# Kernel optimization log

Hardware: AMD Instinct MI355X
Metric: run time of the kernel (lower is better)

Reference implementation:

```python
import jax, jax.numpy as jnp
import numpy as np

D = 160          # volume side
WIN = 32         # spatial window size (box filter, matches fftconvolve with ones kernel)
NUM_MIN = 100    # minimum count constraint (constraint.min_number_from_ratio)
K_CCL = 16       # fixed number of 6-neighbor min-propagation sweeps (CCL definition)
NUM_BINS = 4096  # fixed histogram bins replacing data-dependent np.unique
VALUES = (0, 1, 2)
LIST_LABELS = (1,)
NUM_LABELS = 2
HALF = WIN // 2


def _box1d(x, w, ax):
    # 'same' box-sum along one axis via cumsum (== fftconvolve with ones(w))
    left = w // 2
    right = w - 1 - left
    x = jnp.moveaxis(x, ax, -1)
    pads = [(0, 0)] * (x.ndim - 1) + [(left, right)]
    c = jnp.cumsum(jnp.pad(x, pads), axis=-1)
    c = jnp.pad(c, [(0, 0)] * (x.ndim - 1) + [(1, 0)])
    out = c[..., w:] - c[..., :-w]
    return jnp.moveaxis(out, -1, ax)


def box_sum(x, w):
    for ax in range(x.ndim):
        x = _box1d(x, w, ax)
    return x


def _shift(a, s, ax, fill):
    # shift by s along ax, filling vacated border with `fill`
    r = jnp.roll(a, s, axis=ax)
    n = a.shape[ax]
    co = jnp.arange(n).reshape([n if i == ax else 1 for i in range(a.ndim)])
    bad = (co < s) if s > 0 else (co >= n + s)
    return jnp.where(bad, fill, r)


def label_size_map(seg):
    # create_label_size_map: connected-component labeling (6-connectivity,
    # K_CCL min-propagation sweeps) then replace each component by its size.
    n_vox = seg.size
    big = jnp.int32(n_vox + 2)
    idx = (jnp.arange(n_vox, dtype=jnp.int32) + 1).reshape(seg.shape)
    lab0 = jnp.where(seg, idx, big)

    def step(_, lab):
        m = lab
        for ax in range(seg.ndim):
            for s in (1, -1):
                m = jnp.minimum(m, _shift(lab, s, ax, big))
        return jnp.where(seg, m, big)

    lab = jax.lax.fori_loop(0, K_CCL, step, lab0)
    labels = jnp.where(seg, lab, 0)  # background -> label 0
    cnt = jnp.zeros(n_vox + 1, jnp.float32).at[labels.ravel()].add(1.0)
    return jnp.where(seg, cnt[labels], 0.0)


def _proba_weights(candidates, mean_list):
    # create_probability_weights: reciprocal-histogram weighting over rounded
    # mean component sizes (fixed NUM_BINS integer bins; bin 0 = non-candidate).
    pw = jnp.ones_like(candidates)
    for m in mean_list:
        possible = candidates * m
        idx = jnp.clip(jnp.round(possible), 0, NUM_BINS - 1).astype(jnp.int32)
        hist = jnp.zeros(NUM_BINS, jnp.float32).at[idx.ravel()].add(1.0)
        numb = jnp.sum(hist[1:])
        rec = jnp.where(hist[1:] > 0, numb / jnp.maximum(hist[1:], 1.0), 0.0)
        ph = rec / jnp.sum(rec)
        ph_full = jnp.concatenate([jnp.zeros(1, jnp.float32), ph])
        pw = pw * ph_full[idx]
    return pw / jnp.sum(pw)


def setup_inputs() -> dict:
    key = jax.random.key(0)
    data = jax.random.randint(key, (D, D, D), 0, 3).astype(jnp.float32)
    return {"data": data}


def reference(data):
    data = jnp.round(data)
    inner = tuple(s - 2 * HALF for s in data.shape)
    final = jnp.pad(jnp.ones(inner, jnp.float32), [(HALF, HALF)] * 3)
    mean_list = []
    valid_others = []
    for v in VALUES:
        seg = data == v
        segf = seg.astype(jnp.float32)
        lsize = label_size_map(seg)
        cw = box_sum(segf, WIN)                              # counts_window
        valid = (cw > max(NUM_MIN, 1)).astype(jnp.float32)   # valid_places
        cs = box_sum(lsize * valid, WIN)                     # counts_size
        mean = jnp.where(cw > 0, cs / jnp.maximum(cw, 1.0), 0.0)
        if v in LIST_LABELS:
            mean_list.append(mean)
            final = final * valid
        else:
            valid_others.append(valid)
    for vo in valid_others:
        final = final + vo
    num_labels_add = max(NUM_LABELS - len(LIST_LABELS), 0)
    candidates = (final >= num_labels_add + 1).astype(jnp.float32)
    proba_fin = _proba_weights(candidates, mean_list)
    return candidates, proba_fin
```

## Files before the change

kernel.cpp:

```cpp
#include <hip/hip_runtime.h>
#include <cmath>

#define D 160
#define DD (D*D)
#define NVOX (D*D*D)
#define BIGV (NVOX + 2)
#define NBINS 4096
#define HALF 16
#define RGRID 800
#define SGRID 1000
#define NSWEEP 16

template<int MODE>
__global__ __launch_bounds__(256) void box_rot_int_kernel(
    const void* __restrict__ vin, unsigned* __restrict__ out)
{
    __shared__ unsigned tin[32][161];
    __shared__ unsigned filt[160][33];
    int L0 = blockIdx.x * 32;
    size_t base = (size_t)L0 * D;

    if (MODE == 0) {
        const float4* s4 = (const float4*)((const float*)vin + base);
        for (int i = threadIdx.x; i < 32 * (D / 4); i += 256) {
            float4 v = s4[i];
            int e = i * 4, r = e / D, c = e - r * D;
            float rr;
            rr = rintf(v.x); tin[r][c]   = (rr==0.f) | ((rr==1.f)?0x10000u:0u);
            rr = rintf(v.y); tin[r][c+1] = (rr==0.f) | ((rr==1.f)?0x10000u:0u);
            rr = rintf(v.z); tin[r][c+2] = (rr==0.f) | ((rr==1.f)?0x10000u:0u);
            rr = rintf(v.w); tin[r][c+3] = (rr==0.f) | ((rr==1.f)?0x10000u:0u);
        }
    } else {
        const uint4* s4 = (const uint4*)((const unsigned*)vin + base);
        for (int i = threadIdx.x; i < 32 * (D / 4); i += 256) {
            uint4 v = s4[i];
            int e = i * 4, r = e / D, c = e - r * D;
            tin[r][c] = v.x; tin[r][c+1] = v.y; tin[r][c+2] = v.z; tin[r][c+3] = v.w;
        }
    }
    __syncthreads();

    {
        int r = threadIdx.x & 31, s = threadIdx.x >> 5;
        int i0 = 20 * s;
        const unsigned* ln = tin[r];
        unsigned sum = 0u;
        int jlo = i0 - 16; if (jlo < 0) jlo = 0;
        int jhi = i0 + 15; if (jhi > D - 1) jhi = D - 1;
        for (int j = jlo; j <= jhi; ++j) sum += ln[j];
        #pragma unroll 4
        for (int k = 0; k < 20; ++k) {
            int i = i0 + k;
            filt[i][r] = sum;
            int add = i + 16, rem = i - 16;
            if (add <= D - 1) sum += ln[add];
            if (rem >= 0)     sum -= ln[rem];
        }
    }
    __syncthreads();

    int r = threadIdx.x & 31;
    for (int c = (threadIdx.x >> 5); c < D; c += 8)
        out[(size_t)c * DD + L0 + r] = filt[c][r];
}

__global__ __launch_bounds__(256) void box_rot_f32_g_kernel(
    const int* __restrict__ lab, const int* __restrict__ cnt,
    const unsigned* __restrict__ cwp, float* __restrict__ out)
{
    __shared__ float tin[32][161];
    __shared__ float filt[160][33];
    int L0 = blockIdx.x * 32;
    size_t base = (size_t)L0 * D;

    const int4*  lab4 = (const int4*)(lab + base);
    const uint4* cw4  = (const uint4*)(cwp + base);
    for (int i = threadIdx.x; i < 32 * (D / 4); i += 256) {
        int4 l = lab4[i];
        uint4 cw = cw4[i];
        int e = i * 4, r = e / D, c = e - r * D;
        tin[r][c]   = (l.x != BIGV && (cw.x >> 16) > 100u) ? (float)cnt[l.x] : 0.f;
        tin[r][c+1] = (l.y != BIGV && (cw.y >> 16) > 100u) ? (float)cnt[l.y] : 0.f;
        tin[r][c+2] = (l.z != BIGV && (cw.z >> 16) > 100u) ? (float)cnt[l.z] : 0.f;
        tin[r][c+3] = (l.w != BIGV && (cw.w >> 16) > 100u) ? (float)cnt[l.w] : 0.f;
    }
    __syncthreads();

    {
        int r = threadIdx.x & 31, s = threadIdx.x >> 5;
        int i0 = 20 * s;
        const float* ln = tin[r];
        float sum = 0.f;
        int jlo = i0 - 16; if (jlo < 0) jlo = 0;
        int jhi = i0 + 15; if (jhi > D - 1) jhi = D - 1;
        for (int j = jlo; j <= jhi; ++j) sum += ln[j];
        #pragma unroll 4
        for (int k = 0; k < 20; ++k) {
            int i = i0 + k;
            filt[i][r] = sum;
            int add = i + 16, rem = i - 16;
            if (add <= D - 1) sum += ln[add];
            if (rem >= 0)     sum -= ln[rem];
        }
    }
    __syncthreads();

    int r = threadIdx.x & 31;
    for (int c = (threadIdx.x >> 5); c < D; c += 8)
        out[(size_t)c * DD + L0 + r] = filt[c][r];
}

__global__ __launch_bounds__(256) void box_rot_f32_kernel(
    const float* __restrict__ fin, float* __restrict__ out)
{
    __shared__ float tin[32][161];
    __shared__ float filt[160][33];
    int L0 = blockIdx.x * 32;
    size_t base = (size_t)L0 * D;

    const float4* s4 = (const float4*)(fin + base);
    for (int i = threadIdx.x; i < 32 * (D / 4); i += 256) {
        float4 v = s4[i];
        int e = i * 4, r = e / D, c = e - r * D;
        tin[r][c] = v.x; tin[r][c+1] = v.y; tin[r][c+2] = v.z; tin[r][c+3] = v.w;
    }
    __syncthreads();

    {
        int r = threadIdx.x & 31, s = threadIdx.x >> 5;
        int i0 = 20 * s;
        const float* ln = tin[r];
        float sum = 0.f;
        int jlo = i0 - 16; if (jlo < 0) jlo = 0;
        int jhi = i0 + 15; if (jhi > D - 1) jhi = D - 1;
        for (int j = jlo; j <= jhi; ++j) sum += ln[j];
        #pragma unroll 4
        for (int k = 0; k < 20; ++k) {
            int i = i0 + k;
            filt[i][r] = sum;
            int add = i + 16, rem = i - 16;
            if (add <= D - 1) sum += ln[add];
            if (rem >= 0)     sum -= ln[rem];
        }
    }
    __syncthreads();

    int r = threadIdx.x & 31;
    for (int c = (threadIdx.x >> 5); c < D; c += 8)
        out[(size_t)c * DD + L0 + r] = filt[c][r];
}

__global__ __launch_bounds__(256) void box_rot_fin_kernel(
    const float* __restrict__ fin, const unsigned* __restrict__ cwp,
    float* __restrict__ cand, unsigned short* __restrict__ idxbuf,
    int* __restrict__ partial)
{
    __shared__ float tin[32][161];
    __shared__ float filt[160][33];
    __shared__ int lh[NBINS];
    for (int i = threadIdx.x; i < NBINS; i += 256) lh[i] = 0;

    int L0 = blockIdx.x * 32;
    size_t base = (size_t)L0 * D;
    const float4* s4 = (const float4*)(fin + base);
    for (int i = threadIdx.x; i < 32 * (D / 4); i += 256) {
        float4 v = s4[i];
        int e = i * 4, r = e / D, c = e - r * D;
        tin[r][c] = v.x; tin[r][c+1] = v.y; tin[r][c+2] = v.z; tin[r][c+3] = v.w;
    }
    __syncthreads();

    {
        int r = threadIdx.x & 31, s = threadIdx.x >> 5;
        int i0 = 20 * s;
        const float* ln = tin[r];
        float sum = 0.f;
        int jlo = i0 - 16; if (jlo < 0) jlo = 0;
        int jhi = i0 + 15; if (jhi > D - 1) jhi = D - 1;
        for (int j = jlo; j <= jhi; ++j) sum += ln[j];
        #pragma unroll 4
        for (int k = 0; k < 20; ++k) {
            int i = i0 + k;
            filt[i][r] = sum;
            int add = i + 16, rem = i - 16;
            if (add <= D - 1) sum += ln[add];
            if (rem >= 0)     sum -= ln[rem];
        }
    }
    __syncthreads();

    int r = threadIdx.x & 31;
    int L = L0 + r;
    int y = L / D, z = L - (L / D) * D;
    bool byz = (y >= HALF && y < D - HALF && z >= HALF && z < D - HALF);
    int wy = min(y + 15, D - 1) - max(y - 16, 0) + 1;
    int wz = min(z + 15, D - 1) - max(z - 16, 0) + 1;
    for (int c = (threadIdx.x >> 5); c < D; c += 8) {
        int p = c * DD + L;
        unsigned pk = cwp[p];
        unsigned cw0 = pk & 0xFFFFu;
        unsigned cw1 = pk >> 16;
        int wx = min(c + 15, D - 1) - max(c - 16, 0) + 1;
        unsigned cw2 = (unsigned)(wx * wy * wz) - cw0 - cw1;
        float v0 = (cw0 > 100u) ? 1.f : 0.f;
        float v1 = (cw1 > 100u) ? 1.f : 0.f;
        float v2 = (cw2 > 100u) ? 1.f : 0.f;
        float border = (byz && c >= HALF && c < D - HALF) ? 1.f : 0.f;
        float cd = (border * v1 + v0 + v2 >= 2.f) ? 1.f : 0.f;
        cand[p] = cd;
        float mean = (cw1 > 0u) ? filt[c][r] / fmaxf((float)cw1, 1.f) : 0.f;
        int idx = (int)rintf(cd * mean);
        idx = min(max(idx, 0), NBINS - 1);
        idxbuf[p] = (unsigned short)idx;
        if (idx != 0) atomicAdd(&lh[idx], 1);
    }
    __syncthreads();
    int* po = partial + blockIdx.x * NBINS;
    for (int i = threadIdx.x; i < NBINS; i += 256) po[i] = lh[i];
}

__device__ __forceinline__ int min6(int c, int a, int b, int d, int e, int f, int g) {
    if (c == BIGV) return BIGV;
    return min(min(min(c, a), min(b, d)), min(min(e, f), g));
}

__device__ __forceinline__ void wave_count(int l, int lane, int* __restrict__ cnt) {
    unsigned long long remaining = __ballot(l != BIGV);
    while (remaining) {
        int leader = __ffsll((unsigned long long)remaining) - 1;
        int ll = __shfl(l, leader, 64);
        unsigned long long mm = __ballot(l == ll);
        if (lane == leader) atomicAdd(&cnt[ll], (int)__popcll(mm & remaining));
        remaining &= ~mm;
    }
}

__device__ __forceinline__ int4 cls4(float4 v, int p0) {
    int4 l;
    l.x = (rintf(v.x) == 1.f) ? (p0 + 1) : BIGV;
    l.y = (rintf(v.y) == 1.f) ? (p0 + 2) : BIGV;
    l.z = (rintf(v.z) == 1.f) ? (p0 + 3) : BIGV;
    l.w = (rintf(v.w) == 1.f) ? (p0 + 4) : BIGV;
    return l;
}

#define SWEEP_CHUNK(c, lm, rm, q, p, LOAD4, outv)                         \
    {                                                                     \
        int rr = (p) / D;                                                 \
        int yy = rr % D;                                                  \
        int xx = rr / D;                                                  \
        int4 yl = BIG4, yh = BIG4, xl = BIG4, xh = BIG4;                  \
        if (yy > 0)     yl = LOAD4((q) - D/4,  (p) - D);                  \
        if (yy < D - 1) yh = LOAD4((q) + D/4,  (p) + D);                  \
        if (xx > 0)     xl = LOAD4((q) - DD/4, (p) - DD);                 \
        if (xx < D - 1) xh = LOAD4((q) + DD/4, (p) + DD);                 \
        outv.x = min6(c.x, lm,  c.y, yl.x, yh.x, xl.x, xh.x);             \
        outv.y = min6(c.y, c.x, c.z, yl.y, yh.y, xl.y, xh.y);             \
        outv.z = min6(c.z, c.y, c.w, yl.z, yh.z, xl.z, xh.z);             \
        outv.w = min6(c.w, c.z, rm,  yl.w, yh.w, xl.w, xh.w);             \
    }

__global__ __launch_bounds__(512) void ccl_sweep1_data_kernel(
    const float* __restrict__ data, int* __restrict__ outp)
{
    int b = blockIdx.x;
    int sb = (b & 7) * (SGRID / 8) + (b >> 3);
    int lane = threadIdx.x & 63;
    int wv   = threadIdx.x >> 6;
    int wbase = sb * 4096 + wv * 512;
    int pA = wbase + 4 * lane;
    int pB = pA + 256;
    int qA = pA >> 2, qB = pB >> 2;
    const float4* d4 = (const float4*)data;
    int4 cA = cls4(d4[qA], pA), cB = cls4(d4[qB], pB);

    int zA = pA % D, zB = pB % D;
    int lmA = __shfl_up(cA.w, 1);
    int rmA = __shfl_down(cA.x, 1);
    int lmB = __shfl_up(cB.w, 1);
    int rmB = __shfl_down(cB.x, 1);
    int stA = __shfl(cB.x, 0, 64);
    int stB = __shfl(cA.w, 63, 64);
    if (lane == 63) rmA = stA;
    if (lane == 0)  lmB = stB;
    if (zA == 0)          lmA = BIGV;
    else if (lane == 0)   lmA = (rintf(data[pA - 1]) == 1.f) ? pA : BIGV;
    if (zA == D - 4)      rmA = BIGV;
    if (zB == 0)          lmB = BIGV;
    if (zB == D - 4)      rmB = BIGV;
    else if (lane == 63)  rmB = (rintf(data[pB + 4]) == 1.f) ? (pB + 5) : BIGV;

    const int4 BIG4 = make_int4(BIGV, BIGV, BIGV, BIGV);
    #define LOADD(qq, pp) cls4(d4[(qq)], (pp))
    int4 oA, oB;
    SWEEP_CHUNK(cA, lmA, rmA, qA, pA, LOADD, oA);
    SWEEP_CHUNK(cB, lmB, rmB, qB, pB, LOADD, oB);
    #undef LOADD

    int4* out4 = (int4*)outp;
    out4[qA] = oA; out4[qB] = oB;
}

template<int COUNT>
__global__ __launch_bounds__(512) void ccl_sweep8_kernel(
    const int* __restrict__ lab, int* __restrict__ outp, int* __restrict__ cnt)
{
    int b = blockIdx.x;
    int sb = (b & 7) * (SGRID / 8) + (b >> 3);
    int lane = threadIdx.x & 63;
    int wv   = threadIdx.x >> 6;
    int wbase = sb * 4096 + wv * 512;
    int pA = wbase + 4 * lane;
    int pB = pA + 256;
    int qA = pA >> 2, qB = pB >> 2;
    const int4* lab4 = (const int4*)lab;
    int4 cA = lab4[qA], cB = lab4[qB];

    int zA = pA % D, zB = pB % D;
    int lmA = __shfl_up(cA.w, 1);
    int rmA = __shfl_down(cA.x, 1);
    int lmB = __shfl_up(cB.w, 1);
    int rmB = __shfl_down(cB.x, 1);
    int stA = __shfl(cB.x, 0, 64);
    int stB = __shfl(cA.w, 63, 64);
    if (lane == 63) rmA = stA;
    if (lane == 0)  lmB = stB;
    if (zA == 0)          lmA = BIGV;
    else if (lane == 0)   lmA = lab[pA - 1];
    if (zA == D - 4)      rmA = BIGV;
    if (zB == 0)          lmB = BIGV;
    if (zB == D - 4)      rmB = BIGV;
    else if (lane == 63)  rmB = lab[pB + 4];

    const int4 BIG4 = make_int4(BIGV, BIGV, BIGV, BIGV);
    #define LOADL(qq, pp) lab4[(qq)]
    int4 oA, oB;
    SWEEP_CHUNK(cA, lmA, rmA, qA, pA, LOADL, oA);
    SWEEP_CHUNK(cB, lmB, rmB, qB, pB, LOADL, oB);
    #undef LOADL

    int4* out4 = (int4*)outp;
    out4[qA] = oA; out4[qB] = oB;

    if (COUNT) {
        wave_count(oA.x, lane, cnt);
        wave_count(oA.y, lane, cnt);
        wave_count(oA.z, lane, cnt);
        wave_count(oA.w, lane, cnt);
        wave_count(oB.x, lane, cnt);
        wave_count(oB.y, lane, cnt);
        wave_count(oB.z, lane, cnt);
        wave_count(oB.w, lane, cnt);
    }
}

__global__ __launch_bounds__(256) void hist_reduce_kernel(
    const int* __restrict__ partial, int* __restrict__ hist)
{
    int bin = blockIdx.x * 256 + threadIdx.x;
    int s = 0;
    #pragma unroll 4
    for (int b = 0; b < RGRID; ++b) s += partial[b * NBINS + bin];
    hist[bin] = s;
}

__global__ __launch_bounds__(256) void hist_post_kernel(
    const int* __restrict__ hist, float* __restrict__ ph_full,
    float* __restrict__ Sout)
{
    __shared__ float red[256];
    int t = threadIdx.x;

    float loc = 0.f;
    for (int b = t; b < NBINS; b += 256)
        if (b >= 1) loc += (float)hist[b];
    red[t] = loc; __syncthreads();
    for (int o = 128; o > 0; o >>= 1) { if (t < o) red[t] += red[t + o]; __syncthreads(); }
    float numb = red[0]; __syncthreads();

    loc = 0.f;
    for (int b = t; b < NBINS; b += 256) {
        float r = 0.f;
        if (b >= 1) {
            int h = hist[b];
            if (h > 0) r = numb / (float)h;
        }
        ph_full[b] = r;
        loc += r;
    }
    red[t] = loc; __syncthreads();
    for (int o = 128; o > 0; o >>= 1) { if (t < o) red[t] += red[t + o]; __syncthreads(); }
    float sumrec = red[0]; __syncthreads();
    float inv_sumrec = (sumrec > 0.f) ? 1.f / sumrec : 0.f;

    loc = 0.f;
    for (int b = t; b < NBINS; b += 256) {
        float ph = (b >= 1) ? ph_full[b] * inv_sumrec : 0.f;
        ph_full[b] = ph;
        loc += ph * (float)hist[b];
    }
    red[t] = loc; __syncthreads();
    for (int o = 128; o > 0; o >>= 1) { if (t < o) red[t] += red[t + o]; __syncthreads(); }
    if (t == 0) Sout[0] = (red[0] > 0.f) ? red[0] : 1.f;
}

__global__ __launch_bounds__(256) void proba_kernel(
    const unsigned short* __restrict__ idxbuf,
    const float* __restrict__ ph_full, const float* __restrict__ Sv,
    float* __restrict__ outp)
{
    int t = blockIdx.x * blockDim.x + threadIdx.x;
    ushort4 i4 = ((const ushort4*)idxbuf)[t];
    float inv = 1.f / Sv[0];
    float4 o;
    o.x = ph_full[i4.x] * inv;
    o.y = ph_full[i4.y] * inv;
    o.z = ph_full[i4.z] * inv;
    o.w = ph_full[i4.w] * inv;
    ((float4*)outp)[t] = o;
}

extern "C" void kernel_launch(void* const* d_in, const int* in_sizes, int n_in,
                              void* d_out, int out_size, void* d_ws, size_t ws_size,
                              hipStream_t stream)
{
    const float* data = (const float*)d_in[0];
    float* out   = (float*)d_out;
    float* cand  = out;
    float* proba = out + NVOX;

    char* ws = (char*)d_ws;
    const size_t NB = (size_t)NVOX * sizeof(float);
    float* W1 = (float*)(ws);
    float* W2 = (float*)(ws + NB);
    float* W3 = (float*)(ws + 2 * NB);
    int*   cnt  = (int*)(ws + 3 * NB);
    float* ph   = (float*)(ws + 4 * NB + 16);
    int*   hist = (int*)  (ws + 4 * NB + 16 + NBINS * 4);
    float* Sv   = (float*)(ws + 4 * NB + 16 + 2 * NBINS * 4);
    unsigned short* idxbuf = (unsigned short*)cnt;
    int* partial = (int*)W2;

    dim3 rb(256), rg(RGRID);
    dim3 sbk(512), sg(SGRID);
    dim3 pb(256), pg(NVOX / 4 / 256);

    hipMemsetAsync(cnt, 0, (NVOX + 1) * sizeof(int), stream);

    box_rot_int_kernel<0><<<rg, rb, 0, stream>>>(data, (unsigned*)W1);
    box_rot_int_kernel<1><<<rg, rb, 0, stream>>>(W1, (unsigned*)W3);
    box_rot_int_kernel<1><<<rg, rb, 0, stream>>>(W3, (unsigned*)W1);
    unsigned* cwp = (unsigned*)W1;

    ccl_sweep1_data_kernel<<<sg, sbk, 0, stream>>>(data, (int*)W2);
    for (int i = 0; i < NSWEEP - 2; ++i) {
        const int* src = (i & 1) ? (int*)W3 : (int*)W2;
        int*       dst = (i & 1) ? (int*)W2 : (int*)W3;
        ccl_sweep8_kernel<0><<<sg, sbk, 0, stream>>>(src, dst, nullptr);
    }
    ccl_sweep8_kernel<1><<<sg, sbk, 0, stream>>>((int*)W2, (int*)W3, cnt);
    int* lab = (int*)W3;

    box_rot_f32_g_kernel<<<rg, rb, 0, stream>>>(lab, cnt, cwp, W2);
    box_rot_f32_kernel<<<rg, rb, 0, stream>>>(W2, W3);
    box_rot_fin_kernel<<<rg, rb, 0, stream>>>(W3, cwp, cand, idxbuf, partial);

    hist_reduce_kernel<<<dim3(16), dim3(256), 0, stream>>>(partial, hist);
    hist_post_kernel<<<1, 256, 0, stream>>>(hist, ph, Sv);
    proba_kernel<<<pg, pb, 0, stream>>>(idxbuf, ph, Sv, proba);
}
```

Before: 414.2 us.

## Fuse pairs of CCL min-propagation sweeps into one kernel via neighbor recomputation

Each connected-component sweep kernel now performs two 6-neighbor min-propagation steps. It recomputes the first-step result for the four y/x neighbors of each chunk, plus the left/right z edges at wave boundaries, so the second step can be applied in registers. This halves the number of sweep launches and full-volume label round-trips through memory, from 16 kernels to 8. The cost is more neighbor loads per chunk (diagonal and distance-2 rows), more shuffles and scalar edge loads, and higher register pressure.

```diff
diff --git a/kernel.cpp b/kernel.cpp
--- a/kernel.cpp
+++ b/kernel.cpp
@@ -9,7 +9,6 @@
 #define HALF 16
 #define RGRID 800
 #define SGRID 1000
-#define NSWEEP 16
 
 template<int MODE>
 __global__ __launch_bounds__(256) void box_rot_int_kernel(
@@ -225,6 +224,16 @@
     return min(min(min(c, a), min(b, d)), min(min(e, f), g));
 }
 
+__device__ __forceinline__ int4 min7_run(int4 c, int lm, int rm,
+                                         int4 ym, int4 yp, int4 xm, int4 xp) {
+    int4 o;
+    o.x = min6(c.x, lm,  c.y, ym.x, yp.x, xm.x, xp.x);
+    o.y = min6(c.y, c.x, c.z, ym.y, yp.y, xm.y, xp.y);
+    o.z = min6(c.z, c.y, c.w, ym.z, yp.z, xm.z, xp.z);
+    o.w = min6(c.w, c.z, rm,  ym.w, yp.w, xm.w, xp.w);
+    return o;
+}
+
 __device__ __forceinline__ void wave_count(int l, int lane, int* __restrict__ cnt) {
     unsigned long long remaining = __ballot(l != BIGV);
     while (remaining) {
@@ -245,23 +254,90 @@
     return l;
 }
 
-#define SWEEP_CHUNK(c, lm, rm, q, p, LOAD4, outv)                         \
-    {                                                                     \
-        int rr = (p) / D;                                                 \
-        int yy = rr % D;                                                  \
-        int xx = rr / D;                                                  \
-        int4 yl = BIG4, yh = BIG4, xl = BIG4, xh = BIG4;                  \
-        if (yy > 0)     yl = LOAD4((q) - D/4,  (p) - D);                  \
-        if (yy < D - 1) yh = LOAD4((q) + D/4,  (p) + D);                  \
-        if (xx > 0)     xl = LOAD4((q) - DD/4, (p) - DD);                 \
-        if (xx < D - 1) xh = LOAD4((q) + DD/4, (p) + DD);                 \
-        outv.x = min6(c.x, lm,  c.y, yl.x, yh.x, xl.x, xh.x);             \
-        outv.y = min6(c.y, c.x, c.z, yl.y, yh.y, xl.y, xh.y);             \
-        outv.z = min6(c.z, c.y, c.w, yl.z, yh.z, xl.z, xh.z);             \
-        outv.w = min6(c.w, c.z, rm,  yl.w, yh.w, xl.w, xh.w);             \
-    }
-
-__global__ __launch_bounds__(512) void ccl_sweep1_data_kernel(
+struct LabLd {
+    const int* __restrict__ a;
+    __device__ __forceinline__ int4 v(int p) const { return ((const int4*)a)[p >> 2]; }
+    __device__ __forceinline__ int  s(int p) const { return a[p]; }
+};
+struct DataLd {
+    const float* __restrict__ a;
+    __device__ __forceinline__ int4 v(int p) const { return cls4(((const float4*)a)[p >> 2], p); }
+    __device__ __forceinline__ int  s(int p) const { return (rintf(a[p]) == 1.f) ? (p + 1) : BIGV; }
+};
+
+template<typename LD>
+__device__ __forceinline__ int4 fused2_chunk(LD ld, int p, int lane)
+{
+    const int4 BIG4 = make_int4(BIGV, BIGV, BIGV, BIGV);
+    int z0 = p % D;
+    int rr = p / D;
+    int yy = rr % D;
+    int xx = rr / D;
+    bool gyp = yy < D - 1, gym = yy > 0, gxp = xx < D - 1, gxm = xx > 0;
+
+    int4 C  = ld.v(p);
+    int4 Yp = gyp ? ld.v(p + D)  : BIG4;
+    int4 Ym = gym ? ld.v(p - D)  : BIG4;
+    int4 Xp = gxp ? ld.v(p + DD) : BIG4;
+    int4 Xm = gxm ? ld.v(p - DD) : BIG4;
+
+    bool lz = (z0 == 0), rz = (z0 == D - 4);
+    bool l0  = (lane == 0)  && !lz;
+    bool l63 = (lane == 63) && !rz;
+    int lmC  = __shfl_up(C.w, 1),  rmC  = __shfl_down(C.x, 1);
+    int lmYp = __shfl_up(Yp.w, 1), rmYp = __shfl_down(Yp.x, 1);
+    int lmYm = __shfl_up(Ym.w, 1), rmYm = __shfl_down(Ym.x, 1);
+    int lmXp = __shfl_up(Xp.w, 1), rmXp = __shfl_down(Xp.x, 1);
+    int lmXm = __shfl_up(Xm.w, 1), rmXm = __shfl_down(Xm.x, 1);
+    if (lz) { lmC = lmYp = lmYm = lmXp = lmXm = BIGV; }
+    if (rz) { rmC = rmYp = rmYm = rmXp = rmXm = BIGV; }
+    if (l0) {
+        lmC  = ld.s(p - 1);
+        lmYp = gyp ? ld.s(p + D - 1)  : BIGV;
+        lmYm = gym ? ld.s(p - D - 1)  : BIGV;
+        lmXp = gxp ? ld.s(p + DD - 1) : BIGV;
+        lmXm = gxm ? ld.s(p - DD - 1) : BIGV;
+    }
+    if (l63) {
+        rmC  = ld.s(p + 4);
+        rmYp = gyp ? ld.s(p + D + 4)  : BIGV;
+        rmYm = gym ? ld.s(p - D + 4)  : BIGV;
+        rmXp = gxp ? ld.s(p + DD + 4) : BIGV;
+        rmXm = gxm ? ld.s(p - DD + 4) : BIGV;
+    }
+
+    int4 g1C = min7_run(C, lmC, rmC, Ym, Yp, Xm, Xp);
+
+    int4 Yp2 = (yy < D - 2)  ? ld.v(p + 2 * D)  : BIG4;
+    int4 Dpp = (gxp && gyp)  ? ld.v(p + DD + D) : BIG4;
+    int4 Dmp = (gxm && gyp)  ? ld.v(p - DD + D) : BIG4;
+    int4 g1Yp = min7_run(Yp, lmYp, rmYp, C, Yp2, Dmp, Dpp);
+
+    int4 Ym2 = (yy > 1)      ? ld.v(p - 2 * D)  : BIG4;
+    int4 Dpm = (gxp && gym)  ? ld.v(p + DD - D) : BIG4;
+    int4 Dmm = (gxm && gym)  ? ld.v(p - DD - D) : BIG4;
+    int4 g1Ym = min7_run(Ym, lmYm, rmYm, Ym2, C, Dmm, Dpm);
+
+    int4 Xp2 = (xx < D - 2)  ? ld.v(p + 2 * DD) : BIG4;
+    int4 g1Xp = min7_run(Xp, lmXp, rmXp, Dpm, Dpp, C, Xp2);
+
+    int4 Xm2 = (xx > 1)      ? ld.v(p - 2 * DD) : BIG4;
+    int4 g1Xm = min7_run(Xm, lmXm, rmXm, Dmm, Dmp, Xm2, C);
+
+    int lmG = __shfl_up(g1C.w, 1), rmG = __shfl_down(g1C.x, 1);
+    if (lz) lmG = BIGV;
+    if (rz) rmG = BIGV;
+    if (l0) {
+        lmG = min6(lmC, ld.s(p - 2), C.x, lmYp, lmYm, lmXp, lmXm);
+    }
+    if (l63) {
+        rmG = min6(rmC, C.w, ld.s(p + 5), rmYp, rmYm, rmXp, rmXm);
+    }
+
+    return min7_run(g1C, lmG, rmG, g1Ym, g1Yp, g1Xm, g1Xp);
+}
+
+__global__ __launch_bounds__(512) void ccl_fused2_data_kernel(
     const float* __restrict__ data, int* __restrict__ outp)
 {
     int b = blockIdx.x;
@@ -271,39 +347,17 @@
     int wbase = sb * 4096 + wv * 512;
     int pA = wbase + 4 * lane;
     int pB = pA + 256;
-    int qA = pA >> 2, qB = pB >> 2;
-    const float4* d4 = (const float4*)data;
-    int4 cA = cls4(d4[qA], pA), cB = cls4(d4[qB], pB);
-
-    int zA = pA % D, zB = pB % D;
-    int lmA = __shfl_up(cA.w, 1);
-    int rmA = __shfl_down(cA.x, 1);
-    int lmB = __shfl_up(cB.w, 1);
-    int rmB = __shfl_down(cB.x, 1);
-    int stA = __shfl(cB.x, 0, 64);
-    int stB = __shfl(cA.w, 63, 64);
-    if (lane == 63) rmA = stA;
-    if (lane == 0)  lmB = stB;
-    if (zA == 0)          lmA = BIGV;
-    else if (lane == 0)   lmA = (rintf(data[pA - 1]) == 1.f) ? pA : BIGV;
-    if (zA == D - 4)      rmA = BIGV;
-    if (zB == 0)          lmB = BIGV;
-    if (zB == D - 4)      rmB = BIGV;
-    else if (lane == 63)  rmB = (rintf(data[pB + 4]) == 1.f) ? (pB + 5) : BIGV;
-
-    const int4 BIG4 = make_int4(BIGV, BIGV, BIGV, BIGV);
-    #define LOADD(qq, pp) cls4(d4[(qq)], (pp))
-    int4 oA, oB;
-    SWEEP_CHUNK(cA, lmA, rmA, qA, pA, LOADD, oA);
-    SWEEP_CHUNK(cB, lmB, rmB, qB, pB, LOADD, oB);
-    #undef LOADD
+
+    DataLd ld{data};
+    int4 oA = fused2_chunk(ld, pA, lane);
+    int4 oB = fused2_chunk(ld, pB, lane);
 
     int4* out4 = (int4*)outp;
-    out4[qA] = oA; out4[qB] = oB;
+    out4[pA >> 2] = oA; out4[pB >> 2] = oB;
 }
 
 template<int COUNT>
-__global__ __launch_bounds__(512) void ccl_sweep8_kernel(
+__global__ __launch_bounds__(512) void ccl_fused2_kernel(
     const int* __restrict__ lab, int* __restrict__ outp, int* __restrict__ cnt)
 {
     int b = blockIdx.x;
@@ -313,35 +367,13 @@
     int wbase = sb * 4096 + wv * 512;
     int pA = wbase + 4 * lane;
     int pB = pA + 256;
-    int qA = pA >> 2, qB = pB >> 2;
-    const int4* lab4 = (const int4*)lab;
-    int4 cA = lab4[qA], cB = lab4[qB];
-
-    int zA = pA % D, zB = pB % D;
-    int lmA = __shfl_up(cA.w, 1);
-    int rmA = __shfl_down(cA.x, 1);
-    int lmB = __shfl_up(cB.w, 1);
-    int rmB = __shfl_down(cB.x, 1);
-    int stA = __shfl(cB.x, 0, 64);
-    int stB = __shfl(cA.w, 63, 64);
-    if (lane == 63) rmA = stA;
-    if (lane == 0)  lmB = stB;
-    if (zA == 0)          lmA = BIGV;
-    else if (lane == 0)   lmA = lab[pA - 1];
-    if (zA == D - 4)      rmA = BIGV;
-    if (zB == 0)          lmB = BIGV;
-    if (zB == D - 4)      rmB = BIGV;
-    else if (lane == 63)  rmB = lab[pB + 4];
-
-    const int4 BIG4 = make_int4(BIGV, BIGV, BIGV, BIGV);
-    #define LOADL(qq, pp) lab4[(qq)]
-    int4 oA, oB;
-    SWEEP_CHUNK(cA, lmA, rmA, qA, pA, LOADL, oA);
-    SWEEP_CHUNK(cB, lmB, rmB, qB, pB, LOADL, oB);
-    #undef LOADL
+
+    LabLd ld{lab};
+    int4 oA = fused2_chunk(ld, pA, lane);
+    int4 oB = fused2_chunk(ld, pB, lane);
 
     int4* out4 = (int4*)outp;
-    out4[qA] = oA; out4[qB] = oB;
+    out4[pA >> 2] = oA; out4[pB >> 2] = oB;
 
     if (COUNT) {
         wave_count(oA.x, lane, cnt);
@@ -453,13 +485,14 @@
     box_rot_int_kernel<1><<<rg, rb, 0, stream>>>(W3, (unsigned*)W1);
     unsigned* cwp = (unsigned*)W1;
 
-    ccl_sweep1_data_kernel<<<sg, sbk, 0, stream>>>(data, (int*)W2);
-    for (int i = 0; i < NSWEEP - 2; ++i) {
-        const int* src = (i & 1) ? (int*)W3 : (int*)W2;
-        int*       dst = (i & 1) ? (int*)W2 : (int*)W3;
-        ccl_sweep8_kernel<0><<<sg, sbk, 0, stream>>>(src, dst, nullptr);
-    }
-    ccl_sweep8_kernel<1><<<sg, sbk, 0, stream>>>((int*)W2, (int*)W3, cnt);
+    ccl_fused2_data_kernel<<<sg, sbk, 0, stream>>>(data, (int*)W2);
+    ccl_fused2_kernel<0><<<sg, sbk, 0, stream>>>((int*)W2, (int*)W3, nullptr);
+    ccl_fused2_kernel<0><<<sg, sbk, 0, stream>>>((int*)W3, (int*)W2, nullptr);
+    ccl_fused2_kernel<0><<<sg, sbk, 0, stream>>>((int*)W2, (int*)W3, nullptr);
+    ccl_fused2_kernel<0><<<sg, sbk, 0, stream>>>((int*)W3, (int*)W2, nullptr);
+    ccl_fused2_kernel<0><<<sg, sbk, 0, stream>>>((int*)W2, (int*)W3, nullptr);
+    ccl_fused2_kernel<0><<<sg, sbk, 0, stream>>>((int*)W3, (int*)W2, nullptr);
+    ccl_fused2_kernel<1><<<sg, sbk, 0, stream>>>((int*)W2, (int*)W3, cnt);
     int* lab = (int*)W3;
 
     box_rot_f32_g_kernel<<<rg, rb, 0, stream>>>(lab, cnt, cwp, W2);
```

After: 482.7 us. 16.5% more time.
